# Optimization experiments

Measured on AMD Instinct MI355X. Metric: run time of the kernel, lower is better.

The kernel has to match this reference:

```python
import jax, jax.numpy as jnp
import numpy as np

B, N, D, E, FF, TOP_K = 4, 1024, 1024, 8, 4096, 2

def setup_inputs() -> dict:
    key = jax.random.key(0)
    ks = jax.random.split(key, 6)
    s = lambda k, shape: (jax.random.normal(k, shape, jnp.float32) * 0.02)
    x  = jax.random.normal(ks[0], (B, N, D), jnp.float32)
    Wr = s(ks[1], (E, D))            # router: logits = x @ Wr.T (no bias)
    W1 = s(ks[2], (E, D, FF)); b1 = jnp.zeros((E, FF), jnp.float32)  # fc1
    Wg = s(ks[3], (E, D, FF)); bg = jnp.zeros((E, FF), jnp.float32)  # fc_gate
    W2 = s(ks[4], (E, FF, D)); b2 = jnp.zeros((E, D), jnp.float32)   # fc2
    return {"x": x, "Wr": Wr, "W1": W1, "b1": b1, "Wg": Wg, "bg": bg, "W2": W2, "b2": b2}

def reference(x, Wr, W1, b1, Wg, bg, W2, b2):
    Bb, Nn, Dd = x.shape
    xf = x.reshape(-1, Dd)                      # [T, D]
    T = xf.shape[0]
    logits = xf @ Wr.T                          # [T, E]
    probs = jax.nn.softmax(logits, axis=-1)
    topv, topi = jax.lax.top_k(probs, TOP_K)    # [T, K]
    topv = topv / (topv.sum(-1, keepdims=True) + 1e-6)
    # per-(expert,token) combine weight: comb[t, e] = sum_k topv[t,k] * (topi[t,k]==e)
    comb = jnp.zeros((T, E), x.dtype).at[jnp.arange(T)[:, None], topi].add(topv)
    # scan over experts (fixed small E) to keep memory to one [T, FF] at a time
    def step(acc, p):
        w1, bb1, wg, bbg, w2, bb2, we = p       # we: [T]
        h = xf @ w1 + bb1                       # [T, FF]
        g = xf @ wg + bbg
        out = (jax.nn.silu(g) * h) @ w2 + bb2   # [T, D]
        return acc + we[:, None] * out, None
    acc, _ = jax.lax.scan(step, jnp.zeros((T, Dd), x.dtype), (W1, b1, Wg, bg, W2, b2, comb.T))
    out_final = acc.reshape(Bb, Nn, Dd)
    # load-balance aux loss (computed under no_grad in torch)
    counts = jnp.zeros((E,), x.dtype).at[topi.reshape(-1)].add(1.0)
    frac = counts / (counts.sum() + 1e-6)
    lb = jax.lax.stop_gradient((frac * probs.sum(0)).sum() * E)
    return out_final, lb
```

## Files before the change

kernel.cpp:

```cpp
#include <hip/hip_runtime.h>
#include <hip/hip_bf16.h>
#include <math.h>

#define T_TOK 4096
#define D_DIM 1024
#define E_EXP 8
#define FF_DIM 4096
#define NROWS (T_TOK * 2)
#define MAXT1 40
#define MAXT2 72

typedef unsigned short u16;
typedef unsigned int u32;
typedef __attribute__((ext_vector_type(8))) short bf16x8;
typedef __attribute__((ext_vector_type(4))) float f32x4;
typedef __attribute__((ext_vector_type(2))) unsigned int u32x2;

__device__ __forceinline__ u16 f2bf(float f) {
    union { float f; unsigned u; } v; v.f = f;
    unsigned r = v.u + 0x7FFFu + ((v.u >> 16) & 1u);
    return (u16)(r >> 16);
}

typedef const __attribute__((address_space(1))) u32* gas1_t;
typedef __attribute__((address_space(3))) u32* las3_t;
#define GLOAD16(g, l) __builtin_amdgcn_global_load_lds((gas1_t)(const void*)(g), (las3_t)(void*)(l), 16, 0, 0)
#define MFMA(a, b, c) __builtin_amdgcn_mfma_f32_16x16x32_bf16((a), (b), (c), 0, 0, 0)
#define CVTPK(dst, lo, hi) asm("v_cvt_pk_bf16_f32 %0, %1, %2" : "=v"(dst) : "v"(lo), "v"(hi))
#define CFENCE() asm volatile("" ::: "memory")
#define SIGB(r) (((r) ^ ((r) >> 2)) & 7)


__global__ void k_init(int* cnt, float* probsum) {
    int i = threadIdx.x;
    if (i < E_EXP) { cnt[i] = 0; probsum[i] = 0.f; }
}

__global__ __launch_bounds__(256) void k_router(
    const float* __restrict__ x, const float* __restrict__ Wr,
    int* __restrict__ tok_e, float* __restrict__ tok_w,
    int* __restrict__ cnt, float* __restrict__ probsum)
{
    __shared__ float bp[E_EXP];
    __shared__ int   bc[E_EXP];
    const int tid = threadIdx.x;
    if (tid < E_EXP) { bp[tid] = 0.f; bc[tid] = 0; }
    __syncthreads();
    const int wave = tid >> 6, lane = tid & 63;
    const int t = blockIdx.x * 4 + wave;
    const float* xt = x + (size_t)t * D_DIM;
    float a[E_EXP] = {0.f,0.f,0.f,0.f,0.f,0.f,0.f,0.f};
    for (int j = lane; j < D_DIM; j += 64) {
        float xv = xt[j];
        #pragma unroll
        for (int e = 0; e < E_EXP; e++) a[e] = fmaf(xv, Wr[e * D_DIM + j], a[e]);
    }
    #pragma unroll
    for (int e = 0; e < E_EXP; e++) {
        #pragma unroll
        for (int off = 32; off; off >>= 1) a[e] += __shfl_xor(a[e], off, 64);
    }
    if (lane == 0) {
        float mx = a[0];
        #pragma unroll
        for (int e = 1; e < E_EXP; e++) mx = fmaxf(mx, a[e]);
        float p[E_EXP], s = 0.f;
        #pragma unroll
        for (int e = 0; e < E_EXP; e++) { p[e] = expf(a[e] - mx); s += p[e]; }
        float inv = 1.f / s;
        #pragma unroll
        for (int e = 0; e < E_EXP; e++) { p[e] *= inv; atomicAdd(&bp[e], p[e]); }
        int e0 = 0; float v0 = p[0];
        #pragma unroll
        for (int e = 1; e < E_EXP; e++) if (p[e] > v0) { v0 = p[e]; e0 = e; }
        int e1 = -1; float v1 = -1.f;
        #pragma unroll
        for (int e = 0; e < E_EXP; e++) if (e != e0 && p[e] > v1) { v1 = p[e]; e1 = e; }
        float sv = v0 + v1 + 1e-6f;
        tok_e[2*t] = e0; tok_e[2*t+1] = e1;
        tok_w[2*t] = v0 / sv; tok_w[2*t+1] = v1 / sv;
        atomicAdd(&bc[e0], 1); atomicAdd(&bc[e1], 1);
    }
    __syncthreads();
    if (tid < E_EXP) { atomicAdd(&cnt[tid], bc[tid]); atomicAdd(&probsum[tid], bp[tid]); }
}

__global__ void k_prefix(const int* __restrict__ cnt, const float* __restrict__ probsum,
                         int* __restrict__ basep, int* __restrict__ cursor,
                         float* __restrict__ out_lb,
                         int* __restrict__ nt1, int* __restrict__ te1, int* __restrict__ tm1,
                         int* __restrict__ nt2, int* __restrict__ te2, int* __restrict__ tm2)
{
    if (threadIdx.x == 0) {
        int b = 0; float lb = 0.f;
        for (int e = 0; e < E_EXP; e++) {
            basep[e] = b; b += cnt[e];
            lb += ((float)cnt[e] / (8192.f + 1e-6f)) * probsum[e];
        }
        *out_lb = lb * (float)E_EXP;
        int n1 = 0, n2 = 0;
        for (int e = 0; e < E_EXP; e++) {
            for (int m = 0; m < cnt[e]; m += 256) { te1[n1] = e; tm1[n1] = m; n1++; }
            for (int m = 0; m < cnt[e]; m += 128) { te2[n2] = e; tm2[n2] = m; n2++; }
        }
        *nt1 = n1; *nt2 = n2;
    }
    if (threadIdx.x < E_EXP) cursor[threadIdx.x] = 0;
}

__global__ void k_assign(const int* __restrict__ tok_e, const float* __restrict__ tok_w,
                         const int* __restrict__ basep, int* __restrict__ cursor,
                         int* __restrict__ row_token, int* __restrict__ row_slot,
                         float* __restrict__ row_weight)
{
    int t = blockIdx.x * blockDim.x + threadIdx.x;
    if (t >= T_TOK) return;
    #pragma unroll
    for (int k = 0; k < 2; k++) {
        int e = tok_e[2*t + k];
        int pos = basep[e] + atomicAdd(&cursor[e], 1);
        row_token[pos] = t; row_slot[pos] = k; row_weight[pos] = tok_w[2*t + k];
    }
}

__global__ __launch_bounds__(256) void k_cvt_x(const float* __restrict__ in, u16* __restrict__ out) {
    size_t i = ((size_t)blockIdx.x * 256 + threadIdx.x) * 8;
    f32x4 a = *(const f32x4*)(in + i);
    f32x4 b = *(const f32x4*)(in + i + 4);
    bf16x8 o;
    #pragma unroll
    for (int j = 0; j < 4; j++) { o[j] = (short)f2bf(a[j]); o[j + 4] = (short)f2bf(b[j]); }
    *(bf16x8*)(out + i) = o;
}


__global__ __launch_bounds__(512, 2) void k_pass1(
    const u16* __restrict__ xbf,
    const float* __restrict__ W1, const float* __restrict__ Wg,
    const float* __restrict__ b1v, const float* __restrict__ bgv,
    const int* __restrict__ cnt, const int* __restrict__ basep,
    const int* __restrict__ row_token,
    const int* __restrict__ ntp, const int* __restrict__ te, const int* __restrict__ tm,
    u16* __restrict__ hg)
{
    const int ty = blockIdx.y;
    if (ty >= *ntp) return;
    const int e = te[ty];
    const int m0 = tm[ty];
    const int count = cnt[e];
    const int rbase = basep[e];
    const int n0 = blockIdx.x * 128;

    __shared__ __align__(16) u16 LDS[2 * 32768];

    const int tid = threadIdx.x;
    const int l = tid & 63;
    const int w = tid >> 6;

    const int rb = tid >> 3;
    const int swA = ((tid & 7) ^ ((tid >> 3) & 7)) * 8;
    const u16* sA[4];
    #pragma unroll
    for (int s = 0; s < 4; s++) {
        int g = m0 + rb + s * 64; if (g > count - 1) g = count - 1;
        sA[s] = xbf + (size_t)row_token[rbase + g] * D_DIM + swA;
    }

    const int nq = tid & 31;
    const int kq = tid >> 5;
    const float* pBh = W1 + ((size_t)e * D_DIM + kq * 4) * FF_DIM + n0 + nq * 4;
    const float* pBg = Wg + ((size_t)e * D_DIM + kq * 4) * FF_DIM + n0 + nq * 4;
    const int cW = kq >> 1;
    const int offW = (kq & 1) * 4;
    int wdst[4];
    #pragma unroll
    for (int j = 0; j < 4; j++) {
        const int row = nq * 4 + j;
        wdst[j] = row * 64 + (cW ^ SIGB(row)) * 8 + offW;
    }

    const int wm = w >> 2, wn = w & 3;
    const int fr = l & 15, q = l >> 4;
    const int s7 = fr & 7;

    f32x4 acc_h[8][2], acc_g[8][2];
    const f32x4 z4 = {0.f, 0.f, 0.f, 0.f};
    #pragma unroll
    for (int mf = 0; mf < 8; mf++)
        #pragma unroll
        for (int nf = 0; nf < 2; nf++) { acc_h[mf][nf] = z4; acc_g[mf][nf] = z4; }

    f32x4 vb0, vb1, vb2, vb3;

    #define LOADB1(P, K0) do { \
        const float* p_ = (P) + (size_t)(K0) * FF_DIM; \
        vb0 = *(const f32x4*)(p_); \
        vb1 = *(const f32x4*)(p_ + FF_DIM); \
        vb2 = *(const f32x4*)(p_ + 2 * FF_DIM); \
        vb3 = *(const f32x4*)(p_ + 3 * FF_DIM); \
    } while (0)

    #define CVTW1(BASE) do { \
        _Pragma("unroll") \
        for (int j = 0; j < 4; j++) { \
            u32 lo_, hi_; u32x2 wv_; \
            CVTPK(lo_, vb0[j], vb1[j]); \
            CVTPK(hi_, vb2[j], vb3[j]); \
            wv_.x = lo_; wv_.y = hi_; \
            *(u32x2*)&LDS[(BASE) + wdst[j]] = wv_; \
        } \
    } while (0)

    #define STAGE_A1(B, K0) do { \
        _Pragma("unroll") \
        for (int s = 0; s < 4; s++) \
            GLOAD16(sA[s] + (K0), &LDS[(B) * 32768 + s * 4096 + tid * 8]); \
    } while (0)

    auto COMP = [&](int kk, int ab) {
        const int rsA = ((kk * 4 + q) ^ s7) * 8;
        const int rB0 = wn * 32 + fr, rB1 = wn * 32 + 16 + fr;
        const int cb0 = ((kk * 4 + q) ^ SIGB(rB0)) * 8;
        const int cb1 = ((kk * 4 + q) ^ SIGB(rB1)) * 8;
        bf16x8 bh0 = *(const bf16x8*)&LDS[ab + 16384 + rB0 * 64 + cb0];
        bf16x8 bg0 = *(const bf16x8*)&LDS[ab + 24576 + rB0 * 64 + cb0];
        bf16x8 bh1 = *(const bf16x8*)&LDS[ab + 16384 + rB1 * 64 + cb1];
        bf16x8 bg1 = *(const bf16x8*)&LDS[ab + 24576 + rB1 * 64 + cb1];
        #define LDA1(i) (*(const bf16x8*)&LDS[ab + (wm * 128 + (i) * 16 + fr) * 64 + rsA])
        #define MF4(areg, i) do { \
            __builtin_amdgcn_s_setprio(1); \
            acc_h[i][0] = MFMA(areg, bh0, acc_h[i][0]); \
            acc_h[i][1] = MFMA(areg, bh1, acc_h[i][1]); \
            acc_g[i][0] = MFMA(areg, bg0, acc_g[i][0]); \
            acc_g[i][1] = MFMA(areg, bg1, acc_g[i][1]); \
            __builtin_amdgcn_s_setprio(0); } while (0)
        bf16x8 aA = LDA1(0);
        bf16x8 aB = LDA1(1);
        bf16x8 aC;
        aC = LDA1(2); MF4(aA, 0);
        aA = LDA1(3); MF4(aB, 1);
        aB = LDA1(4); MF4(aC, 2);
        aC = LDA1(5); MF4(aA, 3);
        aA = LDA1(6); MF4(aB, 4);
        aB = LDA1(7); MF4(aC, 5);
        MF4(aA, 6);
        MF4(aB, 7);
        #undef LDA1
        #undef MF4
    };

    const int NT = D_DIM / 64;
    LOADB1(pBh, 0);
    CVTW1(0 + 16384);
    STAGE_A1(0, 0);
    LOADB1(pBg, 0);
    CVTW1(0 + 24576);
    asm volatile("s_waitcnt vmcnt(0) lgkmcnt(0)" ::: "memory");
    __builtin_amdgcn_s_barrier();
    CFENCE();

    int b = 0;
    #pragma unroll 1
    for (int t = 0; t < NT; ++t) {
        const int ab = b * 32768;
        const int nboff = (b ^ 1) * 32768;
        const int kN = (t + 1 < NT ? t + 1 : NT - 1) * 64;
        LOADB1(pBh, kN);
        COMP(0, ab);
        CVTW1(nboff + 16384);
        STAGE_A1(b ^ 1, kN);
        LOADB1(pBg, kN);
        COMP(1, ab);
        CVTW1(nboff + 24576);
        asm volatile("s_waitcnt vmcnt(0) lgkmcnt(0)" ::: "memory");
        __builtin_amdgcn_s_barrier();
        CFENCE();
        b ^= 1;
    }
    asm volatile("s_waitcnt vmcnt(0)" ::: "memory");
    #undef LOADB1
    #undef CVTW1
    #undef STAGE_A1

    const float* b1p = b1v + (size_t)e * FF_DIM + n0;
    const float* bgp = bgv + (size_t)e * FF_DIM + n0;
    #pragma unroll
    for (int mf = 0; mf < 8; mf++) {
        const int rl = wm * 128 + mf * 16 + q * 4;
        #pragma unroll
        for (int r = 0; r < 4; r++) {
            const int g = m0 + rl + r;
            if (g < count) {
                u16* orow = hg + (size_t)(rbase + g) * FF_DIM + n0;
                #pragma unroll
                for (int nf = 0; nf < 2; nf++) {
                    const int col = wn * 32 + nf * 16 + fr;
                    float hv = acc_h[mf][nf][r] + b1p[col];
                    float gv = acc_g[mf][nf][r] + bgp[col];
                    float sig = 1.f / (1.f + expf(-gv));
                    orow[col] = f2bf(gv * sig * hv);
                }
            }
        }
    }
}


__global__ __launch_bounds__(256, 2) void k_pass2(
    const u16* __restrict__ hg,
    const float* __restrict__ W2, const float* __restrict__ b2v,
    const int* __restrict__ cnt, const int* __restrict__ basep,
    const int* __restrict__ row_token, const int* __restrict__ row_slot,
    const float* __restrict__ row_weight,
    const int* __restrict__ ntp, const int* __restrict__ te, const int* __restrict__ tm,
    float* __restrict__ contrib)
{
    const int ty = blockIdx.y;
    if (ty >= *ntp) return;
    const int e = te[ty];
    const int m0 = tm[ty];
    const int count = cnt[e];
    const int rbase = basep[e];
    const int n0 = blockIdx.x * 128;

    __shared__ __align__(16) u16 LDS[2 * 16384];

    const int tid = threadIdx.x;
    const int l = tid & 63;
    const int w = tid >> 6;

    const int rb = tid >> 3;
    const int swA = ((tid & 7) ^ ((tid >> 3) & 7)) * 8;
    const u16* sA[4];
    #pragma unroll
    for (int s = 0; s < 4; s++) {
        int g = m0 + rb + s * 32; if (g > count - 1) g = count - 1;
        sA[s] = hg + (size_t)(rbase + g) * FF_DIM + swA;
    }

    const int nq = tid & 31;
    const int koct = tid >> 5;
    const float* pB = W2 + ((size_t)e * FF_DIM + koct * 8) * D_DIM + n0 + nq * 4;
    int wdst[4];
    #pragma unroll
    for (int j = 0; j < 4; j++) {
        const int row = nq * 4 + j;
        wdst[j] = row * 64 + (koct ^ SIGB(row)) * 8;
    }

    const int wm = w >> 1, wn = w & 1;
    const int fr = l & 15, q = l >> 4;
    const int s7 = fr & 7;

    f32x4 acc[4][4];
    const f32x4 z4 = {0.f, 0.f, 0.f, 0.f};
    #pragma unroll
    for (int mf = 0; mf < 4; mf++)
        #pragma unroll
        for (int nf = 0; nf < 4; nf++) acc[mf][nf] = z4;

    f32x4 vb0, vb1, vb2, vb3;

    #define LOADB2(K0, BT) do { \
        const float* p_ = pB + (size_t)((K0) + (BT) * 4) * D_DIM; \
        vb0 = *(const f32x4*)(p_); \
        vb1 = *(const f32x4*)(p_ + D_DIM); \
        vb2 = *(const f32x4*)(p_ + 2 * D_DIM); \
        vb3 = *(const f32x4*)(p_ + 3 * D_DIM); \
    } while (0)

    #define CVTW2(BASE, BT) do { \
        _Pragma("unroll") \
        for (int j = 0; j < 4; j++) { \
            u32 lo_, hi_; u32x2 wv_; \
            CVTPK(lo_, vb0[j], vb1[j]); \
            CVTPK(hi_, vb2[j], vb3[j]); \
            wv_.x = lo_; wv_.y = hi_; \
            *(u32x2*)&LDS[(BASE) + wdst[j] + (BT) * 4] = wv_; \
        } \
    } while (0)

    #define STAGE_A2(B, K0) do { \
        _Pragma("unroll") \
        for (int s = 0; s < 4; s++) \
            GLOAD16(sA[s] + (K0), &LDS[(B) * 16384 + s * 2048 + tid * 8]); \
    } while (0)

    auto COMP = [&](int kk, int ab) {
        const int rsA = ((kk * 4 + q) ^ s7) * 8;
        bf16x8 a0, a1, a2, a3, bb0, bb1, bb2, bb3;
        {
            const int r0 = wn * 64 + fr, r1 = wn * 64 + 16 + fr;
            const int r2 = wn * 64 + 32 + fr, r3 = wn * 64 + 48 + fr;
            bb0 = *(const bf16x8*)&LDS[ab + 8192 + r0 * 64 + (((kk * 4 + q) ^ SIGB(r0)) * 8)];
            bb1 = *(const bf16x8*)&LDS[ab + 8192 + r1 * 64 + (((kk * 4 + q) ^ SIGB(r1)) * 8)];
            bb2 = *(const bf16x8*)&LDS[ab + 8192 + r2 * 64 + (((kk * 4 + q) ^ SIGB(r2)) * 8)];
            bb3 = *(const bf16x8*)&LDS[ab + 8192 + r3 * 64 + (((kk * 4 + q) ^ SIGB(r3)) * 8)];
        }
        a0 = *(const bf16x8*)&LDS[ab + (wm * 64 + 0 * 16 + fr) * 64 + rsA];
        a1 = *(const bf16x8*)&LDS[ab + (wm * 64 + 1 * 16 + fr) * 64 + rsA];
        a2 = *(const bf16x8*)&LDS[ab + (wm * 64 + 2 * 16 + fr) * 64 + rsA];
        a3 = *(const bf16x8*)&LDS[ab + (wm * 64 + 3 * 16 + fr) * 64 + rsA];
        __builtin_amdgcn_s_setprio(1);
        acc[0][0] = MFMA(a0, bb0, acc[0][0]); acc[0][1] = MFMA(a0, bb1, acc[0][1]);
        acc[0][2] = MFMA(a0, bb2, acc[0][2]); acc[0][3] = MFMA(a0, bb3, acc[0][3]);
        acc[1][0] = MFMA(a1, bb0, acc[1][0]); acc[1][1] = MFMA(a1, bb1, acc[1][1]);
        acc[1][2] = MFMA(a1, bb2, acc[1][2]); acc[1][3] = MFMA(a1, bb3, acc[1][3]);
        acc[2][0] = MFMA(a2, bb0, acc[2][0]); acc[2][1] = MFMA(a2, bb1, acc[2][1]);
        acc[2][2] = MFMA(a2, bb2, acc[2][2]); acc[2][3] = MFMA(a2, bb3, acc[2][3]);
        acc[3][0] = MFMA(a3, bb0, acc[3][0]); acc[3][1] = MFMA(a3, bb1, acc[3][1]);
        acc[3][2] = MFMA(a3, bb2, acc[3][2]); acc[3][3] = MFMA(a3, bb3, acc[3][3]);
        __builtin_amdgcn_s_setprio(0);
    };

    const int NT = FF_DIM / 64;
    LOADB2(0, 0);
    CVTW2(8192, 0);
    STAGE_A2(0, 0);
    LOADB2(0, 1);
    CVTW2(8192, 1);
    asm volatile("s_waitcnt vmcnt(0) lgkmcnt(0)" ::: "memory");
    __builtin_amdgcn_s_barrier();
    CFENCE();

    int b = 0;
    #pragma unroll 1
    for (int t = 0; t < NT; ++t) {
        const int ab = b * 16384;
        const int nboff = (b ^ 1) * 16384;
        const int kN = (t + 1 < NT ? t + 1 : NT - 1) * 64;
        LOADB2(kN, 0);
        COMP(0, ab);
        CVTW2(nboff + 8192, 0);
        STAGE_A2(b ^ 1, kN);
        LOADB2(kN, 1);
        COMP(1, ab);
        CVTW2(nboff + 8192, 1);
        asm volatile("s_waitcnt vmcnt(0) lgkmcnt(0)" ::: "memory");
        __builtin_amdgcn_s_barrier();
        CFENCE();
        b ^= 1;
    }
    asm volatile("s_waitcnt vmcnt(0)" ::: "memory");
    #undef LOADB2
    #undef CVTW2
    #undef STAGE_A2

    const float* b2p = b2v + (size_t)e * D_DIM + n0;
    #pragma unroll
    for (int mf = 0; mf < 4; mf++) {
        const int rl = wm * 64 + mf * 16 + q * 4;
        #pragma unroll
        for (int r = 0; r < 4; r++) {
            const int g = m0 + rl + r;
            if (g < count) {
                const int token = row_token[rbase + g];
                const int slot  = row_slot[rbase + g];
                const float wgt_ = row_weight[rbase + g];
                float* orow = contrib + ((size_t)slot * T_TOK + token) * D_DIM + n0;
                #pragma unroll
                for (int nf = 0; nf < 4; nf++) {
                    const int col = wn * 64 + nf * 16 + fr;
                    orow[col] = wgt_ * (acc[mf][nf][r] + b2p[col]);
                }
            }
        }
    }
}

__global__ void k_combine(const float* __restrict__ contrib, float* __restrict__ out) {
    int i = blockIdx.x * blockDim.x + threadIdx.x;
    const f32x4* c0 = (const f32x4*)contrib;
    const f32x4* c1 = c0 + ((size_t)T_TOK * D_DIM / 4);
    f32x4* o = (f32x4*)out;
    o[i] = c0[i] + c1[i];
}


extern "C" void kernel_launch(void* const* d_in, const int* in_sizes, int n_in,
                              void* d_out, int out_size, void* d_ws, size_t ws_size,
                              hipStream_t stream)
{
    (void)in_sizes; (void)n_in; (void)out_size; (void)ws_size;
    const float* x  = (const float*)d_in[0];
    const float* Wr = (const float*)d_in[1];
    const float* W1 = (const float*)d_in[2];
    const float* b1 = (const float*)d_in[3];
    const float* Wg = (const float*)d_in[4];
    const float* bg = (const float*)d_in[5];
    const float* W2 = (const float*)d_in[6];
    const float* b2 = (const float*)d_in[7];
    float* out = (float*)d_out;

    char* ws = (char*)d_ws;
    u16* xbf = (u16*)ws;             ws += (size_t)T_TOK * D_DIM * sizeof(u16);
    u16* hg = (u16*)ws;              ws += (size_t)NROWS * FF_DIM * sizeof(u16);
    float* contrib = (float*)ws;     ws += (size_t)2 * T_TOK * D_DIM * sizeof(float);
    int* tok_e = (int*)ws;           ws += (size_t)T_TOK * 2 * sizeof(int);
    float* tok_w = (float*)ws;       ws += (size_t)T_TOK * 2 * sizeof(float);
    int* row_token = (int*)ws;       ws += (size_t)NROWS * sizeof(int);
    int* row_slot = (int*)ws;        ws += (size_t)NROWS * sizeof(int);
    float* row_weight = (float*)ws;  ws += (size_t)NROWS * sizeof(float);
    int* cnt = (int*)ws;             ws += 8 * sizeof(int);
    int* basep = (int*)ws;           ws += 8 * sizeof(int);
    int* cursor = (int*)ws;          ws += 8 * sizeof(int);
    float* probsum = (float*)ws;     ws += 8 * sizeof(float);
    int* nt1 = (int*)ws;             ws += sizeof(int);
    int* nt2 = (int*)ws;             ws += sizeof(int);
    int* te1 = (int*)ws;             ws += MAXT1 * sizeof(int);
    int* tm1 = (int*)ws;             ws += MAXT1 * sizeof(int);
    int* te2 = (int*)ws;             ws += MAXT2 * sizeof(int);
    int* tm2 = (int*)ws;             ws += MAXT2 * sizeof(int);

    k_init<<<1, 64, 0, stream>>>(cnt, probsum);
    k_cvt_x<<<(T_TOK * D_DIM / 8) / 256, 256, 0, stream>>>(x, xbf);
    k_router<<<T_TOK / 4, 256, 0, stream>>>(x, Wr, tok_e, tok_w, cnt, probsum);
    k_prefix<<<1, 64, 0, stream>>>(cnt, probsum, basep, cursor, out + (size_t)T_TOK * D_DIM,
                                   nt1, te1, tm1, nt2, te2, tm2);
    k_assign<<<T_TOK / 256, 256, 0, stream>>>(tok_e, tok_w, basep, cursor, row_token, row_slot, row_weight);
    k_pass1<<<dim3(FF_DIM / 128, MAXT1), 512, 0, stream>>>(xbf, W1, Wg, b1, bg, cnt, basep, row_token,
                                                           nt1, te1, tm1, hg);
    k_pass2<<<dim3(D_DIM / 128, MAXT2), 256, 0, stream>>>(hg, W2, b2, cnt, basep, row_token, row_slot, row_weight,
                                                          nt2, te2, tm2, contrib);
    k_combine<<<(T_TOK * D_DIM / 4) / 256, 256, 0, stream>>>(contrib, out);
}
```

Measured before the change: 502.1 us.

## Enlarge pass2 tile to 256 rows with 512 threads and reuse pass1 tile list

The second expert GEMM (hg @ W2) now uses 256-row M tiles with 512 threads (8 waves in a 2x4 layout) instead of 128-row tiles with 256 threads, and reuses the pass1 tile schedule (te1/tm1) instead of building a separate 128-row list. Each fp32 W2 tile is loaded and converted to bf16 once per 256 rows instead of once per 128, halving W2 global traffic and conversion work. The grid axes are swapped so that blocks for the same expert tile run next to each other, and the MFMA loop software-pipelines the A fragment loads. In exchange, per-block LDS grows to 96 KB, each wave holds more accumulators, and tail tiles waste more padded rows.

```diff
diff --git a/kernel.cpp b/kernel.cpp
--- a/kernel.cpp
+++ b/kernel.cpp
@@ -88,8 +88,7 @@
 __global__ void k_prefix(const int* __restrict__ cnt, const float* __restrict__ probsum,
                          int* __restrict__ basep, int* __restrict__ cursor,
                          float* __restrict__ out_lb,
-                         int* __restrict__ nt1, int* __restrict__ te1, int* __restrict__ tm1,
-                         int* __restrict__ nt2, int* __restrict__ te2, int* __restrict__ tm2)
+                         int* __restrict__ nt1, int* __restrict__ te1, int* __restrict__ tm1)
 {
     if (threadIdx.x == 0) {
         int b = 0; float lb = 0.f;
@@ -98,12 +97,10 @@
             lb += ((float)cnt[e] / (8192.f + 1e-6f)) * probsum[e];
         }
         *out_lb = lb * (float)E_EXP;
-        int n1 = 0, n2 = 0;
-        for (int e = 0; e < E_EXP; e++) {
+        int n1 = 0;
+        for (int e = 0; e < E_EXP; e++)
             for (int m = 0; m < cnt[e]; m += 256) { te1[n1] = e; tm1[n1] = m; n1++; }
-            for (int m = 0; m < cnt[e]; m += 128) { te2[n2] = e; tm2[n2] = m; n2++; }
-        }
-        *nt1 = n1; *nt2 = n2;
+        *nt1 = n1;
     }
     if (threadIdx.x < E_EXP) cursor[threadIdx.x] = 0;
 }
@@ -306,7 +303,7 @@
 }
 
 
-__global__ __launch_bounds__(256, 2) void k_pass2(
+__global__ __launch_bounds__(512, 2) void k_pass2(
     const u16* __restrict__ hg,
     const float* __restrict__ W2, const float* __restrict__ b2v,
     const int* __restrict__ cnt, const int* __restrict__ basep,
@@ -315,15 +312,15 @@
     const int* __restrict__ ntp, const int* __restrict__ te, const int* __restrict__ tm,
     float* __restrict__ contrib)
 {
-    const int ty = blockIdx.y;
+    const int ty = blockIdx.x;
     if (ty >= *ntp) return;
     const int e = te[ty];
     const int m0 = tm[ty];
     const int count = cnt[e];
     const int rbase = basep[e];
-    const int n0 = blockIdx.x * 128;
-
-    __shared__ __align__(16) u16 LDS[2 * 16384];
+    const int n0 = blockIdx.y * 128;
+
+    __shared__ __align__(16) u16 LDS[2 * 24576];
 
     const int tid = threadIdx.x;
     const int l = tid & 63;
@@ -334,91 +331,92 @@
     const u16* sA[4];
     #pragma unroll
     for (int s = 0; s < 4; s++) {
-        int g = m0 + rb + s * 32; if (g > count - 1) g = count - 1;
+        int g = m0 + rb + s * 64; if (g > count - 1) g = count - 1;
         sA[s] = hg + (size_t)(rbase + g) * FF_DIM + swA;
     }
 
     const int nq = tid & 31;
-    const int koct = tid >> 5;
-    const float* pB = W2 + ((size_t)e * FF_DIM + koct * 8) * D_DIM + n0 + nq * 4;
+    const int kq = tid >> 5;
+    const float* pB = W2 + ((size_t)e * FF_DIM + kq * 4) * D_DIM + n0 + nq * 4;
+    const int cW = kq >> 1;
+    const int offW = (kq & 1) * 4;
     int wdst[4];
     #pragma unroll
     for (int j = 0; j < 4; j++) {
         const int row = nq * 4 + j;
-        wdst[j] = row * 64 + (koct ^ SIGB(row)) * 8;
-    }
-
-    const int wm = w >> 1, wn = w & 1;
+        wdst[j] = 16384 + row * 64 + (cW ^ SIGB(row)) * 8 + offW;
+    }
+
+    const int wm = w >> 2, wn = w & 3;
     const int fr = l & 15, q = l >> 4;
     const int s7 = fr & 7;
 
-    f32x4 acc[4][4];
+    f32x4 acc[8][2];
     const f32x4 z4 = {0.f, 0.f, 0.f, 0.f};
     #pragma unroll
-    for (int mf = 0; mf < 4; mf++)
-        #pragma unroll
-        for (int nf = 0; nf < 4; nf++) acc[mf][nf] = z4;
+    for (int mf = 0; mf < 8; mf++)
+        #pragma unroll
+        for (int nf = 0; nf < 2; nf++) acc[mf][nf] = z4;
 
     f32x4 vb0, vb1, vb2, vb3;
 
-    #define LOADB2(K0, BT) do { \
-        const float* p_ = pB + (size_t)((K0) + (BT) * 4) * D_DIM; \
+    #define LOADB2(K0) do { \
+        const float* p_ = pB + (size_t)(K0) * D_DIM; \
         vb0 = *(const f32x4*)(p_); \
         vb1 = *(const f32x4*)(p_ + D_DIM); \
         vb2 = *(const f32x4*)(p_ + 2 * D_DIM); \
         vb3 = *(const f32x4*)(p_ + 3 * D_DIM); \
     } while (0)
 
-    #define CVTW2(BASE, BT) do { \
+    #define CVTW2(BASE) do { \
         _Pragma("unroll") \
         for (int j = 0; j < 4; j++) { \
             u32 lo_, hi_; u32x2 wv_; \
             CVTPK(lo_, vb0[j], vb1[j]); \
             CVTPK(hi_, vb2[j], vb3[j]); \
             wv_.x = lo_; wv_.y = hi_; \
-            *(u32x2*)&LDS[(BASE) + wdst[j] + (BT) * 4] = wv_; \
+            *(u32x2*)&LDS[(BASE) + wdst[j]] = wv_; \
         } \
     } while (0)
 
     #define STAGE_A2(B, K0) do { \
         _Pragma("unroll") \
         for (int s = 0; s < 4; s++) \
-            GLOAD16(sA[s] + (K0), &LDS[(B) * 16384 + s * 2048 + tid * 8]); \
+            GLOAD16(sA[s] + (K0), &LDS[(B) * 24576 + s * 4096 + tid * 8]); \
     } while (0)
 
     auto COMP = [&](int kk, int ab) {
         const int rsA = ((kk * 4 + q) ^ s7) * 8;
-        bf16x8 a0, a1, a2, a3, bb0, bb1, bb2, bb3;
-        {
-            const int r0 = wn * 64 + fr, r1 = wn * 64 + 16 + fr;
-            const int r2 = wn * 64 + 32 + fr, r3 = wn * 64 + 48 + fr;
-            bb0 = *(const bf16x8*)&LDS[ab + 8192 + r0 * 64 + (((kk * 4 + q) ^ SIGB(r0)) * 8)];
-            bb1 = *(const bf16x8*)&LDS[ab + 8192 + r1 * 64 + (((kk * 4 + q) ^ SIGB(r1)) * 8)];
-            bb2 = *(const bf16x8*)&LDS[ab + 8192 + r2 * 64 + (((kk * 4 + q) ^ SIGB(r2)) * 8)];
-            bb3 = *(const bf16x8*)&LDS[ab + 8192 + r3 * 64 + (((kk * 4 + q) ^ SIGB(r3)) * 8)];
-        }
-        a0 = *(const bf16x8*)&LDS[ab + (wm * 64 + 0 * 16 + fr) * 64 + rsA];
-        a1 = *(const bf16x8*)&LDS[ab + (wm * 64 + 1 * 16 + fr) * 64 + rsA];
-        a2 = *(const bf16x8*)&LDS[ab + (wm * 64 + 2 * 16 + fr) * 64 + rsA];
-        a3 = *(const bf16x8*)&LDS[ab + (wm * 64 + 3 * 16 + fr) * 64 + rsA];
-        __builtin_amdgcn_s_setprio(1);
-        acc[0][0] = MFMA(a0, bb0, acc[0][0]); acc[0][1] = MFMA(a0, bb1, acc[0][1]);
-        acc[0][2] = MFMA(a0, bb2, acc[0][2]); acc[0][3] = MFMA(a0, bb3, acc[0][3]);
-        acc[1][0] = MFMA(a1, bb0, acc[1][0]); acc[1][1] = MFMA(a1, bb1, acc[1][1]);
-        acc[1][2] = MFMA(a1, bb2, acc[1][2]); acc[1][3] = MFMA(a1, bb3, acc[1][3]);
-        acc[2][0] = MFMA(a2, bb0, acc[2][0]); acc[2][1] = MFMA(a2, bb1, acc[2][1]);
-        acc[2][2] = MFMA(a2, bb2, acc[2][2]); acc[2][3] = MFMA(a2, bb3, acc[2][3]);
-        acc[3][0] = MFMA(a3, bb0, acc[3][0]); acc[3][1] = MFMA(a3, bb1, acc[3][1]);
-        acc[3][2] = MFMA(a3, bb2, acc[3][2]); acc[3][3] = MFMA(a3, bb3, acc[3][3]);
-        __builtin_amdgcn_s_setprio(0);
+        const int rB0 = wn * 32 + fr, rB1 = wn * 32 + 16 + fr;
+        const int cb0 = ((kk * 4 + q) ^ SIGB(rB0)) * 8;
+        const int cb1 = ((kk * 4 + q) ^ SIGB(rB1)) * 8;
+        bf16x8 bb0 = *(const bf16x8*)&LDS[ab + 16384 + rB0 * 64 + cb0];
+        bf16x8 bb1 = *(const bf16x8*)&LDS[ab + 16384 + rB1 * 64 + cb1];
+        #define LDA2(i) (*(const bf16x8*)&LDS[ab + (wm * 128 + (i) * 16 + fr) * 64 + rsA])
+        #define MF2(areg, i) do { \
+            __builtin_amdgcn_s_setprio(1); \
+            acc[i][0] = MFMA(areg, bb0, acc[i][0]); \
+            acc[i][1] = MFMA(areg, bb1, acc[i][1]); \
+            __builtin_amdgcn_s_setprio(0); } while (0)
+        bf16x8 aA = LDA2(0);
+        bf16x8 aB = LDA2(1);
+        bf16x8 aC;
+        aC = LDA2(2); MF2(aA, 0);
+        aA = LDA2(3); MF2(aB, 1);
+        aB = LDA2(4); MF2(aC, 2);
+        aC = LDA2(5); MF2(aA, 3);
+        aA = LDA2(6); MF2(aB, 4);
+        aB = LDA2(7); MF2(aC, 5);
+        MF2(aA, 6);
+        MF2(aB, 7);
+        #undef LDA2
+        #undef MF2
     };
 
     const int NT = FF_DIM / 64;
-    LOADB2(0, 0);
-    CVTW2(8192, 0);
+    LOADB2(0);
+    CVTW2(0);
     STAGE_A2(0, 0);
-    LOADB2(0, 1);
-    CVTW2(8192, 1);
     asm volatile("s_waitcnt vmcnt(0) lgkmcnt(0)" ::: "memory");
     __builtin_amdgcn_s_barrier();
     CFENCE();
@@ -426,16 +424,14 @@
     int b = 0;
     #pragma unroll 1
     for (int t = 0; t < NT; ++t) {
-        const int ab = b * 16384;
-        const int nboff = (b ^ 1) * 16384;
+        const int ab = b * 24576;
+        const int nboff = (b ^ 1) * 24576;
         const int kN = (t + 1 < NT ? t + 1 : NT - 1) * 64;
-        LOADB2(kN, 0);
+        LOADB2(kN);
         COMP(0, ab);
-        CVTW2(nboff + 8192, 0);
+        CVTW2(nboff);
         STAGE_A2(b ^ 1, kN);
-        LOADB2(kN, 1);
         COMP(1, ab);
-        CVTW2(nboff + 8192, 1);
         asm volatile("s_waitcnt vmcnt(0) lgkmcnt(0)" ::: "memory");
         __builtin_amdgcn_s_barrier();
         CFENCE();
@@ -448,8 +444,8 @@
 
     const float* b2p = b2v + (size_t)e * D_DIM + n0;
     #pragma unroll
-    for (int mf = 0; mf < 4; mf++) {
-        const int rl = wm * 64 + mf * 16 + q * 4;
+    for (int mf = 0; mf < 8; mf++) {
+        const int rl = wm * 128 + mf * 16 + q * 4;
         #pragma unroll
         for (int r = 0; r < 4; r++) {
             const int g = m0 + rl + r;
@@ -459,8 +455,8 @@
                 const float wgt_ = row_weight[rbase + g];
                 float* orow = contrib + ((size_t)slot * T_TOK + token) * D_DIM + n0;
                 #pragma unroll
-                for (int nf = 0; nf < 4; nf++) {
-                    const int col = wn * 64 + nf * 16 + fr;
+                for (int nf = 0; nf < 2; nf++) {
+                    const int col = wn * 32 + nf * 16 + fr;
                     orow[col] = wgt_ * (acc[mf][nf][r] + b2p[col]);
                 }
             }
@@ -506,21 +502,18 @@
     int* cursor = (int*)ws;          ws += 8 * sizeof(int);
     float* probsum = (float*)ws;     ws += 8 * sizeof(float);
     int* nt1 = (int*)ws;             ws += sizeof(int);
-    int* nt2 = (int*)ws;             ws += sizeof(int);
     int* te1 = (int*)ws;             ws += MAXT1 * sizeof(int);
     int* tm1 = (int*)ws;             ws += MAXT1 * sizeof(int);
-    int* te2 = (int*)ws;             ws += MAXT2 * sizeof(int);
-    int* tm2 = (int*)ws;             ws += MAXT2 * sizeof(int);
 
     k_init<<<1, 64, 0, stream>>>(cnt, probsum);
     k_cvt_x<<<(T_TOK * D_DIM / 8) / 256, 256, 0, stream>>>(x, xbf);
     k_router<<<T_TOK / 4, 256, 0, stream>>>(x, Wr, tok_e, tok_w, cnt, probsum);
     k_prefix<<<1, 64, 0, stream>>>(cnt, probsum, basep, cursor, out + (size_t)T_TOK * D_DIM,
-                                   nt1, te1, tm1, nt2, te2, tm2);
+                                   nt1, te1, tm1);
     k_assign<<<T_TOK / 256, 256, 0, stream>>>(tok_e, tok_w, basep, cursor, row_token, row_slot, row_weight);
     k_pass1<<<dim3(FF_DIM / 128, MAXT1), 512, 0, stream>>>(xbf, W1, Wg, b1, bg, cnt, basep, row_token,
                                                            nt1, te1, tm1, hg);
-    k_pass2<<<dim3(D_DIM / 128, MAXT2), 256, 0, stream>>>(hg, W2, b2, cnt, basep, row_token, row_slot, row_weight,
-                                                          nt2, te2, tm2, contrib);
+    k_pass2<<<dim3(MAXT1, D_DIM / 128), 512, 0, stream>>>(hg, W2, b2, cnt, basep, row_token, row_slot, row_weight,
+                                                          nt1, te1, tm1, contrib);
     k_combine<<<(T_TOK * D_DIM / 4) / 256, 256, 0, stream>>>(contrib, out);
 }
```

After: 500.8 us. No clear change (-0.3%).
